# Kernel tuning notes

Measured on AMD Instinct MI355X. Metric: run time of the kernel, lower is better.

## Reference

```python
import jax, jax.numpy as jnp
import numpy as np

D0 = 1.0          # constraint distance d
NPEND = 128       # points per pendulum chain
NB = 1024         # number of chains (= batch.max()+1)
LATENT = 256      # latent dim of y
NDIM = 3          # spatial dimensions; x dim = 2*NDIM (pos + vel)


def setup_inputs() -> dict:
    key = jax.random.key(0)
    k1, k2, k3 = jax.random.split(key, 3)
    N = NB * NPEND
    y = jax.random.normal(k1, (N, LATENT), dtype=jnp.float32)
    z = jax.random.normal(k2, (N,), dtype=jnp.float32)
    K = jax.random.normal(k3, (LATENT, 2 * NDIM), dtype=jnp.float32) * 0.05
    batch = (jnp.arange(N, dtype=jnp.int32) // NPEND).astype(jnp.int32)
    return {"y": y, "z": z, "K": K, "batch": batch}


def _delta_r(r):
    # dr[:,0] = r[:,0]; dr[:,i] = r[:,i] - r[:,i-1]
    return jnp.concatenate([r[:, :1], r[:, 1:] - r[:, :-1]], axis=1)


def reference(y, z, K, batch):
    x = y @ K                                  # [N, 6]
    ndim = x.shape[-1] // 2                    # pos_only=False -> 3
    nb = batch.shape[0] // NPEND               # == batch.max()+1 by construction
    r = x[:, :ndim].reshape(nb, -1, ndim)      # [nb, npend, 3]

    dr = _delta_r(r)                           # [nb, npend, 3]
    drnorm = jnp.linalg.norm(dr, axis=-1)      # [nb, npend]
    c = drnorm - D0                            # constraint values
    rn = dr / drnorm[..., None]                # unit chain-difference vectors

    # Jacobian-transpose times constraints, fused over the chain dimension:
    # out[:,i] = c_i * rn_i - c_{i+1} * rn_{i+1};  out[:,-1] = c_{-1} * rn_{-1}
    t = c[..., None] * rn                      # [nb, npend, 3]
    out = t - jnp.concatenate([t[:, 1:], jnp.zeros_like(t[:, :1])], axis=1)

    lam_x = jnp.zeros_like(x).at[:, :ndim].set(out.reshape(-1, ndim))
    lam_y = lam_x @ K.T                        # [N, latent]
    return lam_y
```

## Files before the change

### kernel.cpp

```cpp
#include <hip/hip_runtime.h>

#define NPEND  128
#define LATENT 256
#define KCOLS  6
#define D0_C   1.0f
#define NB_MAX 1024

typedef float f32x4 __attribute__((ext_vector_type(4)));

static __device__ float4 g_r[(size_t)NB_MAX * NPEND];

__global__ __launch_bounds__(256, 4)
void pend_r_kernel(const float* __restrict__ y,
                   const float* __restrict__ K,
                   int ngroups)
{
    const int tid  = threadIdx.x;
    const int lane = tid & 63;
    const int g    = lane >> 4;
    const int sl   = lane & 15;

    const int nwaves = gridDim.x << 2;
    const int wid    = (blockIdx.x << 2) | (tid >> 6);

    const int g0 = wid;
    const int g1 = wid + nwaves;
    const int g2 = wid + 2 * nwaves;
    const int g3 = wid + 3 * nwaves;

    float4 b0[4], b1[4];

    auto issue = [&](int grp, float4 (&b)[4]) {
        const float* p = y + (size_t)(grp * 4 + g) * LATENT + sl * 4;
#pragma unroll
        for (int j = 0; j < 4; ++j)
            b[j] = *(const float4*)(p + j * 64);
    };

    if (g0 < ngroups) issue(g0, b0);
    if (g1 < ngroups) issue(g1, b1);

    float kf0[16], kf1[16], kf2[16];
#pragma unroll
    for (int j = 0; j < 4; ++j)
#pragma unroll
        for (int e = 0; e < 4; ++e) {
            const int k = j * 64 + sl * 4 + e;
            kf0[4 * j + e] = K[k * KCOLS + 0];
            kf1[4 * j + e] = K[k * KCOLS + 1];
            kf2[4 * j + e] = K[k * KCOLS + 2];
        }

    auto consume = [&](const float4 (&b)[4], int grp) {
        float s0 = 0.f, s1 = 0.f, s2 = 0.f;
#pragma unroll
        for (int j = 0; j < 4; ++j) {
            const float4 a = b[j];
            s0 += a.x*kf0[4*j] + a.y*kf0[4*j+1] + a.z*kf0[4*j+2] + a.w*kf0[4*j+3];
            s1 += a.x*kf1[4*j] + a.y*kf1[4*j+1] + a.z*kf1[4*j+2] + a.w*kf1[4*j+3];
            s2 += a.x*kf2[4*j] + a.y*kf2[4*j+1] + a.z*kf2[4*j+2] + a.w*kf2[4*j+3];
        }
#pragma unroll
        for (int off = 8; off >= 1; off >>= 1) {
            s0 += __shfl_xor(s0, off, 16);
            s1 += __shfl_xor(s1, off, 16);
            s2 += __shfl_xor(s2, off, 16);
        }
        if (sl == 0) g_r[grp * 4 + g] = make_float4(s0, s1, s2, 0.f);
    };

    __builtin_amdgcn_sched_barrier(0);
    if (g0 < ngroups) consume(b0, g0);
    if (g2 < ngroups) issue(g2, b0);
    __builtin_amdgcn_sched_barrier(0);
    if (g1 < ngroups) consume(b1, g1);
    if (g3 < ngroups) issue(g3, b1);
    __builtin_amdgcn_sched_barrier(0);
    if (g2 < ngroups) consume(b0, g2);
    if (g3 < ngroups) consume(b1, g3);
}

__global__ __launch_bounds__(256, 4)
void pend_out_kernel(const float* __restrict__ K,
                     float* __restrict__ out,
                     int nrows)
{
    const int tid = threadIdx.x;
    const int hl  = tid & 31;
    const int l0  = hl * 4;

    float ka[8], kb[8], kc[8];
#pragma unroll
    for (int e = 0; e < 4; ++e) {
        ka[e]     = K[(l0 + e) * KCOLS + 0];
        kb[e]     = K[(l0 + e) * KCOLS + 1];
        kc[e]     = K[(l0 + e) * KCOLS + 2];
        ka[4 + e] = K[(l0 + 128 + e) * KCOLS + 0];
        kb[4 + e] = K[(l0 + 128 + e) * KCOLS + 1];
        kc[4 + e] = K[(l0 + 128 + e) * KCOLS + 2];
    }

    const int hh  = blockIdx.x * 8 + (tid >> 5);
    const int nhh = gridDim.x * 8;

    for (int row = hh; row < nrows; row += nhh) {
        const int p = row & (NPEND - 1);

        const float4 rc = g_r[row];
        float px = 0.f, py = 0.f, pz = 0.f;
        if (p > 0) { const float4 rp = g_r[row - 1]; px = rp.x; py = rp.y; pz = rp.z; }

        const float dx = rc.x - px, dy = rc.y - py, dz = rc.z - pz;
        const float n  = sqrtf(dx*dx + dy*dy + dz*dz);
        const float s  = (n - D0_C) / n;
        float ox = s * dx, oy = s * dy, oz = s * dz;

        if (p < NPEND - 1) {
            const float4 rn = g_r[row + 1];
            const float ex = rn.x - rc.x, ey = rn.y - rc.y, ez = rn.z - rc.z;
            const float n2 = sqrtf(ex*ex + ey*ey + ez*ez);
            const float t2 = (n2 - D0_C) / n2;
            ox -= t2 * ex; oy -= t2 * ey; oz -= t2 * ez;
        }

        f32x4 wa, wb;
        wa.x = ox*ka[0] + oy*kb[0] + oz*kc[0];
        wa.y = ox*ka[1] + oy*kb[1] + oz*kc[1];
        wa.z = ox*ka[2] + oy*kb[2] + oz*kc[2];
        wa.w = ox*ka[3] + oy*kb[3] + oz*kc[3];
        wb.x = ox*ka[4] + oy*kb[4] + oz*kc[4];
        wb.y = ox*ka[5] + oy*kb[5] + oz*kc[5];
        wb.z = ox*ka[6] + oy*kb[6] + oz*kc[6];
        wb.w = ox*ka[7] + oy*kb[7] + oz*kc[7];

        float* orow = out + (size_t)row * LATENT;
        __builtin_nontemporal_store(wa, (f32x4*)(orow + l0));
        __builtin_nontemporal_store(wb, (f32x4*)(orow + 128 + l0));
    }
}

extern "C" void kernel_launch(void* const* d_in, const int* in_sizes, int n_in,
                              void* d_out, int out_size, void* d_ws, size_t ws_size,
                              hipStream_t stream) {
    const float* y = (const float*)d_in[0];
    const float* K = (const float*)d_in[2];
    float* out = (float*)d_out;

    int N  = (n_in > 1 && in_sizes) ? in_sizes[1] : (1024 * NPEND);
    int nb = N / NPEND;
    if (nb <= 0) nb = 1024;
    if (nb > NB_MAX) nb = NB_MAX;
    N = nb * NPEND;
    (void)out_size; (void)d_ws; (void)ws_size;

    const int ngroups = N / 4;
    pend_r_kernel<<<2048, 256, 0, stream>>>(y, K, ngroups);
    pend_out_kernel<<<2048, 256, 0, stream>>>(K, out, N);
}
```

Measured before the change: 238.2 us.

## Fuse projection and constraint back-projection into one per-chain kernel with LDS

Replaces the two-kernel pipeline, which round-tripped chain positions through a global scratch array, with one kernel per chain. Each block computes the 128 projected positions into shared memory using double-buffered loads, synchronizes, then each half-wave walks 16 consecutive rows while carrying the previous and current positions in registers to emit the output rows. This removes a kernel launch and the global write/read of intermediates. In exchange the grid shrinks to 1024 blocks with lower occupancy (launch bounds 2), and the load phase and store phase within a block no longer overlap.

```diff
diff --git a/kernel.cpp b/kernel.cpp
--- a/kernel.cpp
+++ b/kernel.cpp
@@ -8,37 +8,35 @@
 
 typedef float f32x4 __attribute__((ext_vector_type(4)));
 
-static __device__ float4 g_r[(size_t)NB_MAX * NPEND];
+__global__ __launch_bounds__(256, 2)
+void pend_fused_kernel(const float* __restrict__ y,
+                       const float* __restrict__ K,
+                       float* __restrict__ out)
+{
+    __shared__ float4 sR[NPEND];
 
-__global__ __launch_bounds__(256, 4)
-void pend_r_kernel(const float* __restrict__ y,
-                   const float* __restrict__ K,
-                   int ngroups)
-{
-    const int tid  = threadIdx.x;
-    const int lane = tid & 63;
-    const int g    = lane >> 4;
-    const int sl   = lane & 15;
+    const int tid = threadIdx.x;
+    const int sl  = tid & 15;
+    const int grp = tid >> 4;
+    const int hl  = tid & 31;
+    const int hw  = tid >> 5;
+    const int l0  = hl * 4;
 
-    const int nwaves = gridDim.x << 2;
-    const int wid    = (blockIdx.x << 2) | (tid >> 6);
-
-    const int g0 = wid;
-    const int g1 = wid + nwaves;
-    const int g2 = wid + 2 * nwaves;
-    const int g3 = wid + 3 * nwaves;
+    const int chain = blockIdx.x;
+    const float* ybase = y   + (size_t)chain * (NPEND * LATENT);
+    float*       obase = out + (size_t)chain * (NPEND * LATENT);
 
     float4 b0[4], b1[4];
 
-    auto issue = [&](int grp, float4 (&b)[4]) {
-        const float* p = y + (size_t)(grp * 4 + g) * LATENT + sl * 4;
-#pragma unroll
-        for (int j = 0; j < 4; ++j)
-            b[j] = *(const float4*)(p + j * 64);
+    auto issueA = [&](int i, float4 (&b)[4]) {
+        const float* p = ybase + (grp * 8 + i) * LATENT + sl * 4;
+        b[0] = *(const float4*)(p);
+        b[1] = *(const float4*)(p + 64);
+        b[2] = *(const float4*)(p + 128);
+        b[3] = *(const float4*)(p + 192);
     };
 
-    if (g0 < ngroups) issue(g0, b0);
-    if (g1 < ngroups) issue(g1, b1);
+    issueA(0, b0);
 
     float kf0[16], kf1[16], kf2[16];
 #pragma unroll
@@ -50,8 +48,18 @@
             kf1[4 * j + e] = K[k * KCOLS + 1];
             kf2[4 * j + e] = K[k * KCOLS + 2];
         }
+    float ka[8], kb[8], kc[8];
+#pragma unroll
+    for (int e = 0; e < 4; ++e) {
+        ka[e]     = K[(l0 + e) * KCOLS + 0];
+        kb[e]     = K[(l0 + e) * KCOLS + 1];
+        kc[e]     = K[(l0 + e) * KCOLS + 2];
+        ka[4 + e] = K[(l0 + 128 + e) * KCOLS + 0];
+        kb[4 + e] = K[(l0 + 128 + e) * KCOLS + 1];
+        kc[4 + e] = K[(l0 + 128 + e) * KCOLS + 2];
+    }
 
-    auto consume = [&](const float4 (&b)[4], int grp) {
+    auto consumeA = [&](int i, const float4 (&b)[4]) {
         float s0 = 0.f, s1 = 0.f, s2 = 0.f;
 #pragma unroll
         for (int j = 0; j < 4; ++j) {
@@ -66,57 +74,50 @@
             s1 += __shfl_xor(s1, off, 16);
             s2 += __shfl_xor(s2, off, 16);
         }
-        if (sl == 0) g_r[grp * 4 + g] = make_float4(s0, s1, s2, 0.f);
+        if (sl == 0) sR[grp * 8 + i] = make_float4(s0, s1, s2, 0.f);
     };
 
     __builtin_amdgcn_sched_barrier(0);
-    if (g0 < ngroups) consume(b0, g0);
-    if (g2 < ngroups) issue(g2, b0);
+    issueA(1, b1);
     __builtin_amdgcn_sched_barrier(0);
-    if (g1 < ngroups) consume(b1, g1);
-    if (g3 < ngroups) issue(g3, b1);
+    consumeA(0, b0);
+    issueA(2, b0);
     __builtin_amdgcn_sched_barrier(0);
-    if (g2 < ngroups) consume(b0, g2);
-    if (g3 < ngroups) consume(b1, g3);
-}
+    consumeA(1, b1);
+    issueA(3, b1);
+    __builtin_amdgcn_sched_barrier(0);
+    consumeA(2, b0);
+    issueA(4, b0);
+    __builtin_amdgcn_sched_barrier(0);
+    consumeA(3, b1);
+    issueA(5, b1);
+    __builtin_amdgcn_sched_barrier(0);
+    consumeA(4, b0);
+    issueA(6, b0);
+    __builtin_amdgcn_sched_barrier(0);
+    consumeA(5, b1);
+    issueA(7, b1);
+    __builtin_amdgcn_sched_barrier(0);
+    consumeA(6, b0);
+    consumeA(7, b1);
 
-__global__ __launch_bounds__(256, 4)
-void pend_out_kernel(const float* __restrict__ K,
-                     float* __restrict__ out,
-                     int nrows)
-{
-    const int tid = threadIdx.x;
-    const int hl  = tid & 31;
-    const int l0  = hl * 4;
+    __syncthreads();
 
-    float ka[8], kb[8], kc[8];
+    const int r0 = hw * 16;
+    float4 rc = sR[r0];
+    float4 rp = (r0 > 0) ? sR[r0 - 1] : make_float4(0.f, 0.f, 0.f, 0.f);
+
 #pragma unroll
-    for (int e = 0; e < 4; ++e) {
-        ka[e]     = K[(l0 + e) * KCOLS + 0];
-        kb[e]     = K[(l0 + e) * KCOLS + 1];
-        kc[e]     = K[(l0 + e) * KCOLS + 2];
-        ka[4 + e] = K[(l0 + 128 + e) * KCOLS + 0];
-        kb[4 + e] = K[(l0 + 128 + e) * KCOLS + 1];
-        kc[4 + e] = K[(l0 + 128 + e) * KCOLS + 2];
-    }
+    for (int i = 0; i < 16; ++i) {
+        const int row = r0 + i;
+        const float4 rn = sR[(row < NPEND - 1) ? row + 1 : row];
 
-    const int hh  = blockIdx.x * 8 + (tid >> 5);
-    const int nhh = gridDim.x * 8;
-
-    for (int row = hh; row < nrows; row += nhh) {
-        const int p = row & (NPEND - 1);
-
-        const float4 rc = g_r[row];
-        float px = 0.f, py = 0.f, pz = 0.f;
-        if (p > 0) { const float4 rp = g_r[row - 1]; px = rp.x; py = rp.y; pz = rp.z; }
-
-        const float dx = rc.x - px, dy = rc.y - py, dz = rc.z - pz;
+        const float dx = rc.x - rp.x, dy = rc.y - rp.y, dz = rc.z - rp.z;
         const float n  = sqrtf(dx*dx + dy*dy + dz*dz);
         const float s  = (n - D0_C) / n;
         float ox = s * dx, oy = s * dy, oz = s * dz;
 
-        if (p < NPEND - 1) {
-            const float4 rn = g_r[row + 1];
+        if (row < NPEND - 1) {
             const float ex = rn.x - rc.x, ey = rn.y - rc.y, ez = rn.z - rc.z;
             const float n2 = sqrtf(ex*ex + ey*ey + ez*ez);
             const float t2 = (n2 - D0_C) / n2;
@@ -133,9 +134,11 @@
         wb.z = ox*ka[6] + oy*kb[6] + oz*kc[6];
         wb.w = ox*ka[7] + oy*kb[7] + oz*kc[7];
 
-        float* orow = out + (size_t)row * LATENT;
+        float* orow = obase + (size_t)row * LATENT;
         __builtin_nontemporal_store(wa, (f32x4*)(orow + l0));
         __builtin_nontemporal_store(wb, (f32x4*)(orow + 128 + l0));
+
+        rp = rc; rc = rn;
     }
 }
 
@@ -150,10 +153,7 @@
     int nb = N / NPEND;
     if (nb <= 0) nb = 1024;
     if (nb > NB_MAX) nb = NB_MAX;
-    N = nb * NPEND;
     (void)out_size; (void)d_ws; (void)ws_size;
 
-    const int ngroups = N / 4;
-    pend_r_kernel<<<2048, 256, 0, stream>>>(y, K, ngroups);
-    pend_out_kernel<<<2048, 256, 0, stream>>>(K, out, N);
+    pend_fused_kernel<<<nb, 256, 0, stream>>>(y, K, out);
 }
```

New measurement: 235.9 us. Within noise of the previous version (-0.9%).
